# Performance work log

Hardware: AMD Instinct MI355X
Metric: run time of the kernel (lower is better)

Reference implementation:

```python
import jax, jax.numpy as jnp
import numpy as np

TOPK = 2
EPS = float(np.finfo(np.float64).eps)


def setup_inputs() -> dict:
    key = jax.random.key(0)
    ks = jax.random.split(key, 6)
    B, D, E = 8192, 1024, 8
    x = jax.random.normal(ks[0], (B, D), dtype=jnp.float32)
    noise = jax.random.normal(ks[1], (B, E), dtype=jnp.float32)
    w_gate = jax.random.normal(ks[2], (D, E), dtype=jnp.float32) * 0.02
    w_noise = jax.random.normal(ks[3], (D, E), dtype=jnp.float32) * 0.02
    W_experts = jax.random.normal(ks[4], (E, D, D), dtype=jnp.float32) * 0.02
    b_experts = jax.random.normal(ks[5], (E, D), dtype=jnp.float32) * 0.02
    return {"x": x, "noise": noise, "w_gate": w_gate, "w_noise": w_noise,
            "W_experts": W_experts, "b_experts": b_experts}


def _gates(x, w_gate, w_noise, noise):
    # noisy top-k gating (Shazeer et al.)
    clean_logits = x @ w_gate                                  # [B, E]
    noise_stddev = jax.nn.softplus(x @ w_noise) + 0.01         # [B, E]
    logits = clean_logits + noise * noise_stddev               # [B, E]
    E = logits.shape[1]
    top_logits, top_idx = jax.lax.top_k(logits, min(TOPK + 1, E))
    top_k_logits = top_logits[:, :TOPK]
    top_k_idx = top_idx[:, :TOPK]
    top_k_gates = jax.nn.softmax(top_k_logits, axis=1)         # [B, k]
    B = logits.shape[0]
    gates = jnp.zeros_like(logits).at[jnp.arange(B)[:, None], top_k_idx].set(top_k_gates)
    return gates                                               # [B, E] sparse


def reference(x, noise, w_gate, w_noise, W_experts, b_experts):
    gates = _gates(x, w_gate, w_noise, noise)                  # [B, E]
    # dense equivalent of sort-based dispatch/combine: zero gates mask out
    # unselected experts, so the combined result is identical math.
    expert_out = jnp.einsum("bd,edh->beh", x, W_experts) + b_experts[None]  # [B, E, D]
    combined = jnp.einsum("be,beh->bh", gates, jnp.exp(expert_out))         # [B, D]
    combined = jnp.where(combined == 0, EPS, combined)
    return jnp.log(combined)
```

## Files before the change

### kernel.cpp

```cpp
#include <hip/hip_runtime.h>
#include <hip/hip_bf16.h>
#include <math.h>

#define B_ROWS 8192
#define DDIM   1024
#define NEXP   8

typedef __attribute__((ext_vector_type(8))) __bf16 bf16x8;
typedef __attribute__((ext_vector_type(4))) float  f32x4;

__device__ __forceinline__ unsigned short f2bf(float f) {
    unsigned u = __builtin_bit_cast(unsigned, f);
    u = (u + 0x7fffu + ((u >> 16) & 1u)) >> 16;
    return (unsigned short)u;
}

#define GLOAD_LDS16(gptr, lptr)                                                \
    __builtin_amdgcn_global_load_lds(                                          \
        (const __attribute__((address_space(1))) unsigned int*)(gptr),         \
        (__attribute__((address_space(3))) unsigned int*)(lptr), 16, 0, 0)

__global__ __launch_bounds__(256) void xconv_kernel(
    const float* __restrict__ x, __hip_bfloat16* __restrict__ xbf)
{
    int i = blockIdx.x * 256 + threadIdx.x;
    const int stride = gridDim.x * 256;
    const int n8 = B_ROWS * DDIM / 8;
    for (; i < n8; i += stride) {
        const float4 f0 = *(const float4*)(x + (size_t)i * 8);
        const float4 f1 = *(const float4*)(x + (size_t)i * 8 + 4);
        union { bf16x8 v; unsigned short u[8]; } pk;
        pk.u[0] = f2bf(f0.x); pk.u[1] = f2bf(f0.y); pk.u[2] = f2bf(f0.z); pk.u[3] = f2bf(f0.w);
        pk.u[4] = f2bf(f1.x); pk.u[5] = f2bf(f1.y); pk.u[6] = f2bf(f1.z); pk.u[7] = f2bf(f1.w);
        *(bf16x8*)((__hip_bfloat16*)xbf + (size_t)i * 8) = pk.v;
    }
}

__global__ __launch_bounds__(256) void wtrans_kernel(
    const float* __restrict__ W, __hip_bfloat16* __restrict__ Wt)
{
    const int e  = blockIdx.z;
    const int k0 = blockIdx.y * 64;
    const int n0 = blockIdx.x * 64;
    __shared__ float st[64][65];

    const int t = threadIdx.x;
    {
        const int kk = t >> 4;
        const int nn = (t & 15) * 4;
#pragma unroll
        for (int p = 0; p < 4; ++p) {
            const int k = p * 16 + kk;
            const float4 v = *(const float4*)(W + (size_t)e * DDIM * DDIM
                                                + (size_t)(k0 + k) * DDIM + n0 + nn);
            st[k][nn + 0] = v.x; st[k][nn + 1] = v.y;
            st[k][nn + 2] = v.z; st[k][nn + 3] = v.w;
        }
    }
    __syncthreads();
    {
        const int wave = t >> 6, lane = t & 63;
        const int nr = lane >> 3, kc = lane & 7;
#pragma unroll
        for (int p = 0; p < 2; ++p) {
            const int n = p * 32 + wave * 8 + nr;
            union { bf16x8 v; unsigned short u[8]; } pk;
#pragma unroll
            for (int j = 0; j < 8; ++j) pk.u[j] = f2bf(st[kc * 8 + j][n]);
            *(bf16x8*)((__hip_bfloat16*)Wt + (size_t)e * DDIM * DDIM
                        + (size_t)(n0 + n) * DDIM + k0 + kc * 8) = pk.v;
        }
    }
}

__global__ __launch_bounds__(256) void gating_kernel(
    const float* __restrict__ x, const float* __restrict__ noise,
    const float* __restrict__ w_gate, const float* __restrict__ w_noise,
    int* __restrict__ counts, int* __restrict__ rowlist, float* __restrict__ gatelist)
{
    __shared__ float wtab[DDIM][16];

    const int t = threadIdx.x;
    {
        const int k0 = t * 4;
#pragma unroll
        for (int kk = 0; kk < 4; ++kk) {
            const float4 g0 = *(const float4*)(w_gate  + (size_t)(k0 + kk) * NEXP);
            const float4 g1 = *(const float4*)(w_gate  + (size_t)(k0 + kk) * NEXP + 4);
            const float4 n0 = *(const float4*)(w_noise + (size_t)(k0 + kk) * NEXP);
            const float4 n1 = *(const float4*)(w_noise + (size_t)(k0 + kk) * NEXP + 4);
            *(float4*)&wtab[k0 + kk][0]  = g0;
            *(float4*)&wtab[k0 + kk][4]  = g1;
            *(float4*)&wtab[k0 + kk][8]  = n0;
            *(float4*)&wtab[k0 + kk][12] = n1;
        }
    }
    __syncthreads();

    const int wave = t >> 6, lane = t & 63;
    const int rs = lane >> 4, c = lane & 15;
    const int row = (blockIdx.x * 4 + wave) * 4 + rs;

    double acc = 0.0;
    const float* xr = x + (size_t)row * DDIM;
#pragma unroll 4
    for (int k4 = 0; k4 < DDIM / 4; ++k4) {
        const float4 xv = *(const float4*)(xr + k4 * 4);
        acc += (double)(xv.x * wtab[k4 * 4 + 0][c]);
        acc += (double)(xv.y * wtab[k4 * 4 + 1][c]);
        acc += (double)(xv.z * wtab[k4 * 4 + 2][c]);
        acc += (double)(xv.w * wtab[k4 * 4 + 3][c]);
    }

    const double vnoise = __shfl_xor(acc, 8);

    double lgv = -1.0e300;
    if (c < 8) {
        const double z  = vnoise;
        const double sp = (z > 30.0) ? z : log1p(exp(z));
        lgv = acc + (double)noise[(size_t)row * NEXP + c] * (sp + 0.01);
    }

    double bv = lgv; int bi = c;
#pragma unroll
    for (int off = 1; off <= 4; off <<= 1) {
        const double ov = __shfl_xor(bv, off);
        const int    oi = __shfl_xor(bi, off);
        if (ov > bv || (ov == bv && oi < bi)) { bv = ov; bi = oi; }
    }
    double b2v = (c == bi) ? -1.0e300 : lgv; int b2i = c;
#pragma unroll
    for (int off = 1; off <= 4; off <<= 1) {
        const double ov = __shfl_xor(b2v, off);
        const int    oi = __shfl_xor(b2i, off);
        if (ov > b2v || (ov == b2v && oi < b2i)) { b2v = ov; b2i = oi; }
    }

    if (c == 0) {
        const double g0 = 1.0 / (1.0 + exp(b2v - bv));
        const double g1 = 1.0 - g0;
        int p0 = atomicAdd(&counts[bi], 1);
        rowlist [bi * B_ROWS + p0] = row;
        gatelist[bi * B_ROWS + p0] = (float)g0;
        int p1 = atomicAdd(&counts[b2i], 1);
        rowlist [b2i * B_ROWS + p1] = row;
        gatelist[b2i * B_ROWS + p1] = (float)g1;
    }
}

__global__ __launch_bounds__(256) void moe_gemm_kernel(
    const __hip_bfloat16* __restrict__ xbf, const __hip_bfloat16* __restrict__ Wt,
    const float* __restrict__ bias,
    const int* __restrict__ counts, const int* __restrict__ rowlist,
    const float* __restrict__ gatelist, float* __restrict__ out)
{
    const int e  = blockIdx.z;
    const int mt = blockIdx.y;
    const int nt = blockIdx.x;
    const int cnt  = counts[e];
    const int row0 = mt * 128;
    if (row0 >= cnt) return;

    __shared__ int   srow[128];
    __shared__ float sgate[128];
    __shared__ __align__(16) unsigned char Alds[128 * 128];
    __shared__ __align__(16) unsigned char Blds[128 * 128];

    const int t = threadIdx.x;
    if (t < 128) {
        const int r = row0 + t;
        srow[t]  = (r < cnt) ? rowlist[e * B_ROWS + r]  : 0;
        sgate[t] = (r < cnt) ? gatelist[e * B_ROWS + r] : 0.0f;
    }
    __syncthreads();

    const int wave = t >> 6, lane = t & 63;
    const int wr = wave >> 1, wc = wave & 1;
    const int l4 = lane >> 4, l16 = lane & 15;
    const int lrow  = lane >> 3;
    const int lchunk = (lane & 7) ^ lrow;

    const char* asrc[4]; const char* bsrc[4];
#pragma unroll
    for (int i = 0; i < 4; ++i) {
        const int r  = wave * 32 + i * 8 + lrow;
        asrc[i] = (const char*)xbf + 2 * ((size_t)srow[r] * DDIM + lchunk * 8);
        const int gn = nt * 128 + wave * 32 + i * 8 + lrow;
        bsrc[i] = (const char*)Wt  + 2 * ((size_t)e * DDIM * DDIM + (size_t)gn * DDIM + lchunk * 8);
    }

    f32x4 acc[4][4];
#pragma unroll
    for (int m = 0; m < 4; ++m)
#pragma unroll
        for (int n = 0; n < 4; ++n) acc[m][n] = (f32x4){0.f, 0.f, 0.f, 0.f};

    for (int kt = 0; kt < DDIM / 64; ++kt) {
        const int koff = kt * 128;
#pragma unroll
        for (int i = 0; i < 4; ++i) {
            GLOAD_LDS16(asrc[i] + koff, Alds + (wave * 32 + i * 8) * 128);
            GLOAD_LDS16(bsrc[i] + koff, Blds + (wave * 32 + i * 8) * 128);
        }
        asm volatile("s_waitcnt vmcnt(0)" ::: "memory");
        __syncthreads();

#pragma unroll
        for (int ks = 0; ks < 2; ++ks) {
            bf16x8 af[4], bfr[4];
#pragma unroll
            for (int m = 0; m < 4; ++m) {
                const int row = wr * 64 + m * 16 + l16;
                af[m] = *(const bf16x8*)(Alds + row * 128 + ((ks * 64 + l4 * 16) ^ ((row & 7) << 4)));
            }
#pragma unroll
            for (int n = 0; n < 4; ++n) {
                const int rn = wc * 64 + n * 16 + l16;
                bfr[n] = *(const bf16x8*)(Blds + rn * 128 + ((ks * 64 + l4 * 16) ^ ((rn & 7) << 4)));
            }
#pragma unroll
            for (int m = 0; m < 4; ++m)
#pragma unroll
                for (int n = 0; n < 4; ++n)
                    acc[m][n] = __builtin_amdgcn_mfma_f32_16x16x32_bf16(af[m], bfr[n], acc[m][n], 0, 0, 0);
        }
        __syncthreads();
    }

#pragma unroll
    for (int m = 0; m < 4; ++m) {
#pragma unroll
        for (int n = 0; n < 4; ++n) {
#pragma unroll
            for (int j = 0; j < 4; ++j) {
                const int R = wr * 64 + m * 16 + l4 * 4 + j;
                if (row0 + R < cnt) {
                    const int   brow = srow[R];
                    const float g    = sgate[R];
                    const int   h    = nt * 128 + wc * 64 + n * 16 + l16;
                    const float v    = g * __expf(acc[m][n][j] + bias[e * DDIM + h]);
                    unsafeAtomicAdd(out + (size_t)brow * DDIM + h, v);
                }
            }
        }
    }
}

__global__ __launch_bounds__(256) void logeps_kernel(float* __restrict__ o, int n4)
{
    const float EPSF = 2.220446049250313e-16f;
    int i = blockIdx.x * blockDim.x + threadIdx.x;
    const int stride = gridDim.x * blockDim.x;
    float4* p = (float4*)o;
    for (; i < n4; i += stride) {
        float4 v = p[i];
        v.x = __logf(v.x == 0.0f ? EPSF : v.x);
        v.y = __logf(v.y == 0.0f ? EPSF : v.y);
        v.z = __logf(v.z == 0.0f ? EPSF : v.z);
        v.w = __logf(v.w == 0.0f ? EPSF : v.w);
        p[i] = v;
    }
}

extern "C" void kernel_launch(void* const* d_in, const int* in_sizes, int n_in,
                              void* d_out, int out_size, void* d_ws, size_t ws_size,
                              hipStream_t stream)
{
    const float* x       = (const float*)d_in[0];
    const float* noise   = (const float*)d_in[1];
    const float* w_gate  = (const float*)d_in[2];
    const float* w_noise = (const float*)d_in[3];
    const float* W       = (const float*)d_in[4];
    const float* bias    = (const float*)d_in[5];
    float* out = (float*)d_out;

    char* ws = (char*)d_ws;
    int*   counts   = (int*)ws;
    int*   rowlist  = (int*)(ws + 1024);
    float* gatelist = (float*)(ws + 1024 + NEXP * B_ROWS * 4);
    __hip_bfloat16* xbf = (__hip_bfloat16*)(ws + (1u << 20));
    __hip_bfloat16* Wt  = (__hip_bfloat16*)(ws + (1u << 20) + (16u << 20));

    hipMemsetAsync(counts, 0, 64, stream);
    hipMemsetAsync(d_out, 0, (size_t)out_size * sizeof(float), stream);

    xconv_kernel<<<1024, 256, 0, stream>>>(x, xbf);
    wtrans_kernel<<<dim3(16, 16, NEXP), 256, 0, stream>>>(W, Wt);
    gating_kernel<<<B_ROWS / 16, 256, 0, stream>>>(x, noise, w_gate, w_noise,
                                                   counts, rowlist, gatelist);

    dim3 grid(NEXP, B_ROWS / 128, NEXP);
    moe_gemm_kernel<<<grid, 256, 0, stream>>>(xbf, Wt, bias, counts, rowlist, gatelist, out);

    logeps_kernel<<<2048, 256, 0, stream>>>(out, out_size / 4);
}
```

Baseline: 368.1 us.

## Replace atomic output accumulation with rank-split plain stores into two buffers

Each token's second-choice expert entry is tagged with a rank bit, so the GEMM epilogue writes plain stores into one of two output buffers instead of doing float atomic adds. The final log kernel sums both buffers before taking the log, and the memset of the output is dropped. The grid is also reordered so experts vary faster than row tiles, which changes block scheduling. The cost is one extra 32 MB buffer read, and correctness depends on every row being written exactly once per rank, which holds because top-2 picks always assign both ranks.

Result: faster. 323.5 us (-12.1%).

```diff
diff --git a/kernel.cpp b/kernel.cpp
--- a/kernel.cpp
+++ b/kernel.cpp
@@ -143,7 +143,7 @@
         rowlist [bi * B_ROWS + p0] = row;
         gatelist[bi * B_ROWS + p0] = (float)g0;
         int p1 = atomicAdd(&counts[b2i], 1);
-        rowlist [b2i * B_ROWS + p1] = row;
+        rowlist [b2i * B_ROWS + p1] = (int)((unsigned)row | 0x80000000u);
         gatelist[b2i * B_ROWS + p1] = (float)g1;
     }
 }
@@ -152,16 +152,17 @@
     const __hip_bfloat16* __restrict__ xbf, const __hip_bfloat16* __restrict__ Wt,
     const float* __restrict__ bias,
     const int* __restrict__ counts, const int* __restrict__ rowlist,
-    const float* __restrict__ gatelist, float* __restrict__ out)
-{
-    const int e  = blockIdx.z;
-    const int mt = blockIdx.y;
+    const float* __restrict__ gatelist, float* __restrict__ out, float* __restrict__ out2)
+{
     const int nt = blockIdx.x;
+    const int e  = blockIdx.y;
+    const int mt = blockIdx.z;
     const int cnt  = counts[e];
     const int row0 = mt * 128;
     if (row0 >= cnt) return;
 
     __shared__ int   srow[128];
+    __shared__ unsigned char srank[128];
     __shared__ float sgate[128];
     __shared__ __align__(16) unsigned char Alds[128 * 128];
     __shared__ __align__(16) unsigned char Blds[128 * 128];
@@ -169,7 +170,9 @@
     const int t = threadIdx.x;
     if (t < 128) {
         const int r = row0 + t;
-        srow[t]  = (r < cnt) ? rowlist[e * B_ROWS + r]  : 0;
+        const unsigned er = (r < cnt) ? (unsigned)rowlist[e * B_ROWS + r] : 0u;
+        srow[t]  = (int)(er & 0x7fffffffu);
+        srank[t] = (unsigned char)(er >> 31);
         sgate[t] = (r < cnt) ? gatelist[e * B_ROWS + r] : 0.0f;
     }
     __syncthreads();
@@ -239,26 +242,31 @@
                     const float g    = sgate[R];
                     const int   h    = nt * 128 + wc * 64 + n * 16 + l16;
                     const float v    = g * __expf(acc[m][n][j] + bias[e * DDIM + h]);
-                    unsafeAtomicAdd(out + (size_t)brow * DDIM + h, v);
+                    float* dst = srank[R] ? out2 : out;
+                    dst[(size_t)brow * DDIM + h] = v;
                 }
             }
         }
     }
 }
 
-__global__ __launch_bounds__(256) void logeps_kernel(float* __restrict__ o, int n4)
+__global__ __launch_bounds__(256) void logeps_kernel(
+    float* __restrict__ o, const float* __restrict__ o2, int n4)
 {
     const float EPSF = 2.220446049250313e-16f;
     int i = blockIdx.x * blockDim.x + threadIdx.x;
     const int stride = gridDim.x * blockDim.x;
     float4* p = (float4*)o;
+    const float4* q = (const float4*)o2;
     for (; i < n4; i += stride) {
-        float4 v = p[i];
-        v.x = __logf(v.x == 0.0f ? EPSF : v.x);
-        v.y = __logf(v.y == 0.0f ? EPSF : v.y);
-        v.z = __logf(v.z == 0.0f ? EPSF : v.z);
-        v.w = __logf(v.w == 0.0f ? EPSF : v.w);
-        p[i] = v;
+        float4 a = p[i];
+        const float4 b = q[i];
+        a.x += b.x; a.y += b.y; a.z += b.z; a.w += b.w;
+        a.x = __logf(a.x == 0.0f ? EPSF : a.x);
+        a.y = __logf(a.y == 0.0f ? EPSF : a.y);
+        a.z = __logf(a.z == 0.0f ? EPSF : a.z);
+        a.w = __logf(a.w == 0.0f ? EPSF : a.w);
+        p[i] = a;
     }
 }
 
@@ -280,17 +288,18 @@
     float* gatelist = (float*)(ws + 1024 + NEXP * B_ROWS * 4);
     __hip_bfloat16* xbf = (__hip_bfloat16*)(ws + (1u << 20));
     __hip_bfloat16* Wt  = (__hip_bfloat16*)(ws + (1u << 20) + (16u << 20));
+    float* out2 = (float*)(ws + (1u << 20) + (32u << 20));
 
     hipMemsetAsync(counts, 0, 64, stream);
-    hipMemsetAsync(d_out, 0, (size_t)out_size * sizeof(float), stream);
 
     xconv_kernel<<<1024, 256, 0, stream>>>(x, xbf);
     wtrans_kernel<<<dim3(16, 16, NEXP), 256, 0, stream>>>(W, Wt);
     gating_kernel<<<B_ROWS / 16, 256, 0, stream>>>(x, noise, w_gate, w_noise,
                                                    counts, rowlist, gatelist);
 
-    dim3 grid(NEXP, B_ROWS / 128, NEXP);
-    moe_gemm_kernel<<<grid, 256, 0, stream>>>(xbf, Wt, bias, counts, rowlist, gatelist, out);
-
-    logeps_kernel<<<2048, 256, 0, stream>>>(out, out_size / 4);
-}
+    dim3 grid(NEXP , NEXP , B_ROWS / 128 );
+    moe_gemm_kernel<<<grid, 256, 0, stream>>>(xbf, Wt, bias, counts, rowlist, gatelist,
+                                              out, out2);
+
+    logeps_kernel<<<2048, 256, 0, stream>>>(out, out2, out_size / 4);
+}
```
